# Optimization experiments

Measured on AMD Instinct MI355X. Metric: run time of the kernel, lower is better.

## Reference

```python
import jax, jax.numpy as jnp
import numpy as np

D_MODEL = 768
D_STATE = 128
EXPAND = 2
D_CONV = 4
HEADDIM = 48
D_INNER = EXPAND * D_MODEL            # 1536
NHEADS = D_INNER // HEADDIM           # 32
CONV_DIM = D_INNER + 2 * D_STATE      # 1792 (ngroups=1)
D_IN_PROJ = 2 * D_INNER + 2 * D_STATE + NHEADS  # 3360
EPS = 1e-5


def setup_inputs() -> dict:
    key = jax.random.key(0)
    ks = jax.random.split(key, 8)
    B, L = 2, 1024
    x = jax.random.normal(ks[0], (B, L, D_MODEL), dtype=jnp.float32)
    in_proj_w = jax.random.normal(ks[1], (D_IN_PROJ, D_MODEL), dtype=jnp.float32) * 0.02
    conv_w = jax.random.normal(ks[2], (CONV_DIM, D_CONV), dtype=jnp.float32) * 0.1
    conv_b = jnp.zeros((CONV_DIM,), dtype=jnp.float32)
    # dt init as in Mamba2: dt ~ logspace[1e-3, 1e-1], dt_bias = softplus^-1(dt)
    u = jax.random.uniform(ks[3], (NHEADS,), dtype=jnp.float32)
    dt = jnp.exp(u * (np.log(0.1) - np.log(0.001)) + np.log(0.001))
    dt_bias = jnp.log(jnp.expm1(dt))
    # A in [1, 16]
    A_log = jnp.log(jax.random.uniform(ks[4], (NHEADS,), dtype=jnp.float32) * 15.0 + 1.0)
    D = jnp.ones((NHEADS,), dtype=jnp.float32)
    rms_w = jnp.ones((D_INNER,), dtype=jnp.float32)
    out_proj_w = jax.random.normal(ks[5], (D_MODEL, D_INNER), dtype=jnp.float32) * 0.02
    ln_w = jnp.ones((D_MODEL,), dtype=jnp.float32)
    ln_b = jnp.zeros((D_MODEL,), dtype=jnp.float32)
    return {"x": x, "in_proj_w": in_proj_w, "conv_w": conv_w, "conv_b": conv_b,
            "dt_bias": dt_bias, "A_log": A_log, "D": D, "rms_w": rms_w,
            "out_proj_w": out_proj_w, "ln_w": ln_w, "ln_b": ln_b}


def _mamba_block(x, in_proj_w, conv_w, conv_b, dt_bias, A_log, D, rms_w, out_proj_w, ln_w, ln_b):
    B, L, _ = x.shape
    zxbcdt = jnp.einsum('bld,ed->ble', x, in_proj_w)          # (B,L,D_IN_PROJ)
    z = zxbcdt[..., :D_INNER]                                  # gate
    xBC = zxbcdt[..., D_INNER:D_INNER + CONV_DIM]              # (B,L,CONV_DIM)
    dt = jax.nn.softplus(zxbcdt[..., -NHEADS:] + dt_bias)      # (B,L,H)

    # causal depthwise conv1d (kernel 4) + SiLU
    xp = jnp.pad(xBC, ((0, 0), (D_CONV - 1, 0), (0, 0)))
    conv = conv_b
    for k in range(D_CONV):
        conv = conv + xp[:, k:k + L, :] * conv_w[:, k]
    xBC = jax.nn.silu(conv)

    xs = xBC[..., :D_INNER].reshape(B, L, NHEADS, HEADDIM)     # (B,L,H,P)
    Bm = xBC[..., D_INNER:D_INNER + D_STATE]                   # (B,L,N)
    Cm = xBC[..., D_INNER + D_STATE:]                          # (B,L,N)

    A = -jnp.exp(A_log)                                        # (H,)
    dA = jnp.exp(dt * A)                                       # (B,L,H)
    xdt = xs * dt[..., None]                                   # (B,L,H,P)

    def step(h, inp):
        dA_t, xdt_t, B_t, C_t = inp                            # (B,H),(B,H,P),(B,N),(B,N)
        h = h * dA_t[:, :, None, None] + jnp.einsum('bhp,bn->bhpn', xdt_t, B_t)
        y_t = jnp.einsum('bhpn,bn->bhp', h, C_t)
        return h, y_t

    h0 = jnp.zeros((B, NHEADS, HEADDIM, D_STATE), dtype=x.dtype)
    _, ys = jax.lax.scan(step, h0,
                         (dA.transpose(1, 0, 2), xdt.transpose(1, 0, 2, 3),
                          Bm.transpose(1, 0, 2), Cm.transpose(1, 0, 2)))
    y = ys.transpose(1, 0, 2, 3) + D[None, None, :, None] * xs  # (B,L,H,P)
    y = y.reshape(B, L, D_INNER)

    # gated RMSNorm: rmsnorm(y * silu(z)) * rms_w
    yg = y * jax.nn.silu(z)
    yg = yg * jax.lax.rsqrt(jnp.mean(yg * yg, axis=-1, keepdims=True) + EPS) * rms_w
    out = jnp.einsum('ble,de->bld', yg, out_proj_w)

    # residual + LayerNorm
    r = out + x
    mu = jnp.mean(r, axis=-1, keepdims=True)
    var = jnp.mean((r - mu) ** 2, axis=-1, keepdims=True)
    return (r - mu) * jax.lax.rsqrt(var + EPS) * ln_w + ln_b


def reference(x, in_proj_w, conv_w, conv_b, dt_bias, A_log, D, rms_w, out_proj_w, ln_w, ln_b):
    return _mamba_block(x, in_proj_w, conv_w, conv_b, dt_bias, A_log, D, rms_w,
                        out_proj_w, ln_w, ln_b)
```

## Files before the change

### kernel.cpp

```cpp
#include <hip/hip_runtime.h>
#include <math.h>

#define BDIM 2
#define LLEN 1024
#define DMODEL 768
#define DINNER 1536
#define DSTATE 128
#define NH 32
#define HD 48
#define CONVD 1792
#define DPROJ 3360
#define DPROJP 3456
#define QCH 128
#define NCH 8
#define ROWS (BDIM*LLEN)

typedef unsigned short ushort_t;
typedef __attribute__((ext_vector_type(4))) short short4v;
typedef __attribute__((ext_vector_type(8))) short short8v;
typedef __attribute__((ext_vector_type(4))) float floatx4;

#define OFF_ZX   0ull
#define OFF_XBC  3538944ull
#define OFF_DT   5373952ull
#define OFF_LA   5439488ull
#define OFF_SC   5505024ull
#define OFF_Y    8650752ull
#define OFF_PP   11796480ull
#define OFF_CBT  11797504ull
#define OFF_BTBF 12059648ull
#define OFF_XPT  12190720ull

__device__ __forceinline__ ushort_t f2bf(float f) {
  union { float f; unsigned int u; } v; v.f = f;
  return (ushort_t)((v.u + 0x7FFFu + ((v.u >> 16) & 1u)) >> 16);
}
__device__ __forceinline__ float bf2f(short s) {
  union { unsigned int u; float f; } v; v.u = ((unsigned int)(ushort_t)s) << 16;
  return v.f;
}

#define GLOAD_LDS16(gptr, lptr) \
  __builtin_amdgcn_global_load_lds( \
      (const __attribute__((address_space(1))) void*)(gptr), \
      (__attribute__((address_space(3))) void*)(lptr), 16, 0, 0)

__global__ __launch_bounds__(256) void convert_in_kernel(
    const float* __restrict__ x, const float* __restrict__ w,
    ushort_t* __restrict__ xbf, ushort_t* __restrict__ ipwbf) {
  const int blk = blockIdx.x;
  if (blk < 768) {
    const int i = blk * 256 + threadIdx.x;
    const float4 a = ((const float4*)x)[i * 2];
    const float4 b = ((const float4*)x)[i * 2 + 1];
    short8v o;
    o[0] = (short)f2bf(a.x); o[1] = (short)f2bf(a.y);
    o[2] = (short)f2bf(a.z); o[3] = (short)f2bf(a.w);
    o[4] = (short)f2bf(b.x); o[5] = (short)f2bf(b.y);
    o[6] = (short)f2bf(b.z); o[7] = (short)f2bf(b.w);
    *(short8v*)(xbf + (size_t)i * 8) = o;
  } else {
    const int i = (blk - 768) * 256 + threadIdx.x;
    const int row = i / (DMODEL / 8);
    short8v o;
    if (row < DPROJ) {
      const float4 a = ((const float4*)w)[i * 2];
      const float4 b = ((const float4*)w)[i * 2 + 1];
      o[0] = (short)f2bf(a.x); o[1] = (short)f2bf(a.y);
      o[2] = (short)f2bf(a.z); o[3] = (short)f2bf(a.w);
      o[4] = (short)f2bf(b.x); o[5] = (short)f2bf(b.y);
      o[6] = (short)f2bf(b.z); o[7] = (short)f2bf(b.w);
    } else {
      for (int j = 0; j < 8; j++) o[j] = 0;
    }
    *(short8v*)(ipwbf + (size_t)i * 8) = o;
  }
}

__global__ __launch_bounds__(256) void convert_bf16_kernel(
    const float* __restrict__ in, ushort_t* __restrict__ out, int n8) {
  const int i = blockIdx.x * 256 + threadIdx.x;
  if (i >= n8) return;
  const float4 a = ((const float4*)in)[i * 2];
  const float4 b = ((const float4*)in)[i * 2 + 1];
  short8v o;
  o[0] = (short)f2bf(a.x); o[1] = (short)f2bf(a.y);
  o[2] = (short)f2bf(a.z); o[3] = (short)f2bf(a.w);
  o[4] = (short)f2bf(b.x); o[5] = (short)f2bf(b.y);
  o[6] = (short)f2bf(b.z); o[7] = (short)f2bf(b.w);
  *(short8v*)(out + (size_t)i * 8) = o;
}

__global__ __launch_bounds__(256) void gemm_bf16_bfout(
    const ushort_t* __restrict__ A, const ushort_t* __restrict__ B,
    ushort_t* __restrict__ C, int M, int N, int K) {
  __shared__ __align__(16) ushort_t As[128 * 32];
  __shared__ __align__(16) ushort_t Bs[128 * 32];
  const int tid = threadIdx.x, lane = tid & 63, w = tid >> 6;
  const int wm = (w >> 1) * 64, wn = (w & 1) * 64;
  const int m0 = blockIdx.y * 128, n0 = blockIdx.x * 128;
  floatx4 acc[4][4];
#pragma unroll
  for (int i = 0; i < 4; i++)
#pragma unroll
    for (int j = 0; j < 4; j++) acc[i][j] = (floatx4){0.f, 0.f, 0.f, 0.f};
  const int srow = tid >> 2, skc = (tid & 3) * 8;
  const int kk = (lane >> 4) * 8, fr = lane & 15;
  for (int k0 = 0; k0 < K; k0 += 32) {
#pragma unroll
    for (int i = 0; i < 2; i++) {
      GLOAD_LDS16(A + (size_t)(m0 + i * 64 + srow) * K + k0 + skc,
                  As + (i * 64 + srow) * 32 + skc);
      GLOAD_LDS16(B + (size_t)(n0 + i * 64 + srow) * K + k0 + skc,
                  Bs + (i * 64 + srow) * 32 + skc);
    }
    __syncthreads();
    short8v a[4], bv[4];
#pragma unroll
    for (int mr = 0; mr < 4; mr++)
      a[mr] = *(const short8v*)(As + (wm + mr * 16 + fr) * 32 + kk);
#pragma unroll
    for (int nc = 0; nc < 4; nc++)
      bv[nc] = *(const short8v*)(Bs + (wn + nc * 16 + fr) * 32 + kk);
#pragma unroll
    for (int mr = 0; mr < 4; mr++)
#pragma unroll
      for (int nc = 0; nc < 4; nc++)
        acc[mr][nc] = __builtin_amdgcn_mfma_f32_16x16x32_bf16(
            a[mr], bv[nc], acc[mr][nc], 0, 0, 0);
    __syncthreads();
  }
  const int crow = (lane >> 4) * 4;
#pragma unroll
  for (int mr = 0; mr < 4; mr++)
#pragma unroll
    for (int nc = 0; nc < 4; nc++)
#pragma unroll
      for (int j = 0; j < 4; j++)
        C[(size_t)(m0 + wm + mr * 16 + crow + j) * N + n0 + wn + nc * 16 + fr] =
            f2bf(acc[mr][nc][j]);
}

__global__ __launch_bounds__(256) void gemm_bf16_n64(
    const ushort_t* __restrict__ A, const ushort_t* __restrict__ B,
    float* __restrict__ C, int M, int N, int K) {
  __shared__ __align__(16) ushort_t As[128 * 32];
  __shared__ __align__(16) ushort_t Bs[64 * 32];
  const int tid = threadIdx.x, lane = tid & 63, w = tid >> 6;
  const int wm = (w >> 1) * 64, wn = (w & 1) * 32;
  const int m0 = blockIdx.y * 128, n0 = blockIdx.x * 64;
  floatx4 acc[4][2];
#pragma unroll
  for (int i = 0; i < 4; i++)
#pragma unroll
    for (int j = 0; j < 2; j++) acc[i][j] = (floatx4){0.f, 0.f, 0.f, 0.f};
  const int srow = tid >> 2, skc = (tid & 3) * 8;
  const int kk = (lane >> 4) * 8, fr = lane & 15;
  for (int k0 = 0; k0 < K; k0 += 32) {
#pragma unroll
    for (int i = 0; i < 2; i++)
      GLOAD_LDS16(A + (size_t)(m0 + i * 64 + srow) * K + k0 + skc,
                  As + (i * 64 + srow) * 32 + skc);
    GLOAD_LDS16(B + (size_t)(n0 + srow) * K + k0 + skc, Bs + srow * 32 + skc);
    __syncthreads();
    short8v a[4], bv[2];
#pragma unroll
    for (int mr = 0; mr < 4; mr++)
      a[mr] = *(const short8v*)(As + (wm + mr * 16 + fr) * 32 + kk);
#pragma unroll
    for (int nc = 0; nc < 2; nc++)
      bv[nc] = *(const short8v*)(Bs + (wn + nc * 16 + fr) * 32 + kk);
#pragma unroll
    for (int mr = 0; mr < 4; mr++)
#pragma unroll
      for (int nc = 0; nc < 2; nc++)
        acc[mr][nc] = __builtin_amdgcn_mfma_f32_16x16x32_bf16(
            a[mr], bv[nc], acc[mr][nc], 0, 0, 0);
    __syncthreads();
  }
  const int crow = (lane >> 4) * 4;
#pragma unroll
  for (int mr = 0; mr < 4; mr++)
#pragma unroll
    for (int nc = 0; nc < 2; nc++)
#pragma unroll
      for (int j = 0; j < 4; j++)
        C[(size_t)(m0 + wm + mr * 16 + crow + j) * N + n0 + wn + nc * 16 + fr] =
            acc[mr][nc][j];
}

__global__ __launch_bounds__(256) void conv_dt_kernel(
    const ushort_t* __restrict__ zxb, const float* __restrict__ conv_w,
    const float* __restrict__ conv_b, const float* __restrict__ dt_bias,
    ushort_t* __restrict__ xbcb, float* __restrict__ dtbuf) {
  const int row = blockIdx.x;
  const int t = row % LLEN;
  const int tid = threadIdx.x;
  for (int g = tid; g < CONVD / 4; g += 256) {
    const int c = g * 4;
    const float4 cb = *(const float4*)&conv_b[c];
    float acc0 = cb.x, acc1 = cb.y, acc2 = cb.z, acc3 = cb.w;
    float4 cw[4];
#pragma unroll
    for (int j = 0; j < 4; j++) cw[j] = *(const float4*)&conv_w[(c + j) * 4];
#pragma unroll
    for (int k = 0; k < 4; k++) {
      if (t - 3 + k >= 0) {
        const short4v v = *(const short4v*)&zxb[(size_t)(row - 3 + k) * DPROJP + DINNER + c];
        acc0 += bf2f(v[0]) * ((const float*)&cw[0])[k];
        acc1 += bf2f(v[1]) * ((const float*)&cw[1])[k];
        acc2 += bf2f(v[2]) * ((const float*)&cw[2])[k];
        acc3 += bf2f(v[3]) * ((const float*)&cw[3])[k];
      }
    }
    short4v o;
    o[0] = (short)f2bf(acc0 / (1.f + expf(-acc0)));
    o[1] = (short)f2bf(acc1 / (1.f + expf(-acc1)));
    o[2] = (short)f2bf(acc2 / (1.f + expf(-acc2)));
    o[3] = (short)f2bf(acc3 / (1.f + expf(-acc3)));
    *(short4v*)&xbcb[(size_t)row * CONVD + c] = o;
  }
  if (tid < NH) {
    const float v = bf2f(zxb[(size_t)row * DPROJP + (DPROJ - NH) + tid]) + dt_bias[tid];
    dtbuf[row * NH + tid] = (v > 20.f) ? v : log1pf(expf(v));
  }
}

__global__ __launch_bounds__(128) void cumsum_kernel(
    const float* __restrict__ dtb, const float* __restrict__ A_log,
    float* __restrict__ la2, float* __restrict__ Pp) {
  const int c = blockIdx.x, h = blockIdx.y, b = blockIdx.z;
  const int tid = threadIdx.x, lane = tid & 63;
  const int row = b * LLEN + c * QCH + tid;
  __shared__ float s0;
  float v = dtb[(size_t)row * NH + h];
#pragma unroll
  for (int off = 1; off < 64; off <<= 1) {
    const float u = __shfl_up(v, off, 64);
    if (lane >= off) v += u;
  }
  if (tid == 63) s0 = v;
  __syncthreads();
  if (tid >= 64) v += s0;
  const float la2v = -expf(A_log[h]) * v * 1.44269504088896f;
  la2[(size_t)row * NH + h] = la2v;
  if (tid == 127) Pp[(b * NH + h) * NCH + c] = exp2f(la2v);
}

__global__ __launch_bounds__(256) void prep_bt_kernel(
    const ushort_t* __restrict__ xbcb, ushort_t* __restrict__ BTbf) {
  const int bc = blockIdx.x;
  const int b = bc / NCH, c = bc % NCH;
  const int row0 = b * LLEN + c * QCH;
  const int tid = threadIdx.x;
  __shared__ ushort_t lb[128][136];
  for (int idx = tid; idx < 128 * 32; idx += 256) {
    const int t = idx >> 5, f4 = (idx & 31) * 4;
    const short4v v = *(const short4v*)&xbcb[(size_t)(row0 + t) * CONVD + DINNER + f4];
    *(short4v*)&lb[t][f4] = v;
  }
  __syncthreads();
  for (int idx = tid; idx < 128 * 16; idx += 256) {
    const int n = idx & 127, t0 = (idx >> 7) * 8;
    short8v o;
#pragma unroll
    for (int j = 0; j < 8; j++) o[j] = lb[t0 + j][n];
    *(short8v*)&BTbf[(size_t)(bc * 128 + n) * 128 + t0] = o;
  }
}

__global__ __launch_bounds__(256) void prep_x_kernel(
    const ushort_t* __restrict__ xbcb, const float* __restrict__ dtb,
    ushort_t* __restrict__ XpT) {
  const int c = blockIdx.x, h = blockIdx.y, b = blockIdx.z;
  const int row0 = b * LLEN + c * QCH;
  const int tid = threadIdx.x;
  __shared__ ushort_t xl[128][56];
  __shared__ float dts[128];
  if (tid < 128) dts[tid] = dtb[(size_t)(row0 + tid) * NH + h];
  __syncthreads();
  for (int idx = tid; idx < 128 * 12; idx += 256) {
    const int r = idx / 12, f4 = (idx % 12) * 4;
    const short4v v = *(const short4v*)&xbcb[(size_t)(row0 + r) * CONVD + h * HD + f4];
    const float d = dts[r];
    short4v o;
    o[0] = (short)f2bf(bf2f(v[0]) * d); o[1] = (short)f2bf(bf2f(v[1]) * d);
    o[2] = (short)f2bf(bf2f(v[2]) * d); o[3] = (short)f2bf(bf2f(v[3]) * d);
    *(short4v*)&xl[r][f4] = o;
  }
  __syncthreads();
  const size_t base = ((size_t)(b * NCH + c) * NH + h) * HD * 128;
  for (int idx = tid; idx < 48 * 16; idx += 256) {
    const int p = idx % 48, t0 = (idx / 48) * 8;
    short8v o;
#pragma unroll
    for (int j = 0; j < 8; j++) o[j] = xl[t0 + j][p];
    *(short8v*)&XpT[base + (size_t)p * 128 + t0] = o;
  }
}

__global__ __launch_bounds__(256) void cbt_kernel(
    const ushort_t* __restrict__ xbcb, float* __restrict__ CBt) {
  const int bc = blockIdx.x;
  const int b = bc / NCH, c = bc % NCH;
  const int row0 = b * LLEN + c * QCH;
  const int tid = threadIdx.x, lane = tid & 63, w = tid >> 6;
  const int wm = w * 32;
  const int fr = lane & 15, kk = (lane >> 4) * 8;
  floatx4 acc[2][8];
#pragma unroll
  for (int i = 0; i < 2; i++)
#pragma unroll
    for (int j = 0; j < 8; j++) acc[i][j] = (floatx4){0.f, 0.f, 0.f, 0.f};
  for (int ki = 0; ki < 4; ki++) {
    const int kg = ki * 32 + kk;
    short8v a[2], bv[8];
#pragma unroll
    for (int mt = 0; mt < 2; mt++)
      a[mt] = *(const short8v*)&xbcb[(size_t)(row0 + wm + mt * 16 + fr) * CONVD +
                                     DINNER + DSTATE + kg];
#pragma unroll
    for (int nt = 0; nt < 8; nt++)
      bv[nt] = *(const short8v*)&xbcb[(size_t)(row0 + nt * 16 + fr) * CONVD +
                                      DINNER + kg];
#pragma unroll
    for (int mt = 0; mt < 2; mt++)
#pragma unroll
      for (int nt = 0; nt < 8; nt++)
        acc[mt][nt] = __builtin_amdgcn_mfma_f32_16x16x32_bf16(
            a[mt], bv[nt], acc[mt][nt], 0, 0, 0);
  }
  const int crow = (lane >> 4) * 4;
#pragma unroll
  for (int mt = 0; mt < 2; mt++)
#pragma unroll
    for (int nt = 0; nt < 8; nt++)
#pragma unroll
      for (int j = 0; j < 4; j++)
        CBt[(size_t)(bc * 128 + wm + mt * 16 + crow + j) * 128 + nt * 16 + fr] =
            acc[mt][nt][j];
}

__global__ __launch_bounds__(256) void stateA_kernel(
    const ushort_t* __restrict__ XpT, const ushort_t* __restrict__ BTbf,
    const float* __restrict__ la2, float* __restrict__ Sc) {
  const int c = blockIdx.x, h = blockIdx.y, b = blockIdx.z;
  const int bc = b * NCH + c, bh = b * NH + h;
  const int row0 = b * LLEN + c * QCH;
  const int tid = threadIdx.x, lane = tid & 63, w = tid >> 6;
  __shared__ float ew[128];
  const float laL = la2[(size_t)(row0 + 127) * NH + h];
  if (tid < 128) ew[tid] = exp2f(laL - la2[(size_t)(row0 + tid) * NH + h]);
  __syncthreads();
  const int wn = w * 32;
  const int fr = lane & 15, kk = (lane >> 4) * 8;
  const size_t xbase = ((size_t)bc * NH + h) * HD * 128;
  floatx4 acc[3][2];
#pragma unroll
  for (int i = 0; i < 3; i++)
#pragma unroll
    for (int j = 0; j < 2; j++) acc[i][j] = (floatx4){0.f, 0.f, 0.f, 0.f};
  for (int ki = 0; ki < 4; ki++) {
    const int kg = ki * 32 + kk;
    short8v a[3], bv[2];
#pragma unroll
    for (int mt = 0; mt < 3; mt++) {
      const short8v raw = *(const short8v*)&XpT[xbase + (size_t)(mt * 16 + fr) * 128 + kg];
      short8v s;
#pragma unroll
      for (int e = 0; e < 8; e++) s[e] = (short)f2bf(bf2f(raw[e]) * ew[kg + e]);
      a[mt] = s;
    }
#pragma unroll
    for (int nt = 0; nt < 2; nt++)
      bv[nt] = *(const short8v*)&BTbf[(size_t)(bc * 128 + wn + nt * 16 + fr) * 128 + kg];
#pragma unroll
    for (int mt = 0; mt < 3; mt++)
#pragma unroll
      for (int nt = 0; nt < 2; nt++)
        acc[mt][nt] = __builtin_amdgcn_mfma_f32_16x16x32_bf16(
            a[mt], bv[nt], acc[mt][nt], 0, 0, 0);
  }
  const int crow = (lane >> 4) * 4;
  float* sc = Sc + (size_t)(bh * NCH + c) * (HD * DSTATE);
#pragma unroll
  for (int mt = 0; mt < 3; mt++)
#pragma unroll
    for (int nt = 0; nt < 2; nt++)
#pragma unroll
      for (int j = 0; j < 4; j++)
        sc[(size_t)(mt * 16 + crow + j) * 128 + wn + nt * 16 + fr] = acc[mt][nt][j];
}

__global__ __launch_bounds__(256) void chunk_combine_kernel(
    float* __restrict__ Sc, const float* __restrict__ Pp) {
  const int bh = blockIdx.x;
  const int tid = threadIdx.x;
  for (int e = tid; e < HD * DSTATE; e += 256) {
    float hv = 0.f;
#pragma unroll
    for (int c = 0; c < NCH; c++) {
      const size_t idx = ((size_t)(bh * NCH + c)) * HD * DSTATE + e;
      const float sv = Sc[idx];
      Sc[idx] = hv;
      hv = hv * Pp[bh * NCH + c] + sv;
    }
  }
}

__global__ __launch_bounds__(256) void ykernel(
    const float* __restrict__ CBt, const ushort_t* __restrict__ XpT,
    const ushort_t* __restrict__ xbcb, const float* __restrict__ Hc,
    const float* __restrict__ la2, float* __restrict__ y) {
  const int c = blockIdx.x, h = blockIdx.y, b = blockIdx.z;
  const int bc = b * NCH + c, bh = b * NH + h;
  const int row0 = b * LLEN + c * QCH;
  const int tid = threadIdx.x, lane = tid & 63, w = tid >> 6;
  __shared__ float laL[128], el[128];
  if (tid < 128) {
    const float v = la2[(size_t)(row0 + tid) * NH + h];
    laL[tid] = v; el[tid] = exp2f(v);
  }
  __syncthreads();
  const int wm = w * 32;
  const int fr = lane & 15, kk = (lane >> 4) * 8;
  const size_t xbase = ((size_t)bc * NH + h) * HD * 128;
  const float* hin = Hc + (size_t)(bh * NCH + c) * (HD * DSTATE);
  floatx4 acc[2][3];
#pragma unroll
  for (int i = 0; i < 2; i++)
#pragma unroll
    for (int j = 0; j < 3; j++) acc[i][j] = (floatx4){0.f, 0.f, 0.f, 0.f};

  for (int ki = 0; ki < 4; ki++) {
    const int kg = ki * 32 + kk;
    short8v a[2], bv[3];
#pragma unroll
    for (int mt = 0; mt < 2; mt++) {
      const int t = wm + mt * 16 + fr;
      const float lt = laL[t];
      const float* cb = &CBt[(size_t)(bc * 128 + t) * 128 + kg];
      const float4 u0 = *(const float4*)cb;
      const float4 u1 = *(const float4*)(cb + 4);
      const float f[8] = {u0.x, u0.y, u0.z, u0.w, u1.x, u1.y, u1.z, u1.w};
      short8v s;
#pragma unroll
      for (int e = 0; e < 8; e++) {
        const int sidx = kg + e;
        const float m = (t >= sidx) ? exp2f(lt - laL[sidx]) : 0.f;
        s[e] = (short)f2bf(f[e] * m);
      }
      a[mt] = s;
    }
#pragma unroll
    for (int nt = 0; nt < 3; nt++)
      bv[nt] = *(const short8v*)&XpT[xbase + (size_t)(nt * 16 + fr) * 128 + kg];
#pragma unroll
    for (int mt = 0; mt < 2; mt++)
#pragma unroll
      for (int nt = 0; nt < 3; nt++)
        acc[mt][nt] = __builtin_amdgcn_mfma_f32_16x16x32_bf16(
            a[mt], bv[nt], acc[mt][nt], 0, 0, 0);
  }
  for (int ki = 0; ki < 4; ki++) {
    const int kg = ki * 32 + kk;
    short8v a[2], bv[3];
#pragma unroll
    for (int mt = 0; mt < 2; mt++) {
      const int t = wm + mt * 16 + fr;
      const float scl = el[t];
      const short8v raw = *(const short8v*)&xbcb[(size_t)(row0 + t) * CONVD +
                                                 DINNER + DSTATE + kg];
      short8v s;
#pragma unroll
      for (int e = 0; e < 8; e++) s[e] = (short)f2bf(bf2f(raw[e]) * scl);
      a[mt] = s;
    }
#pragma unroll
    for (int nt = 0; nt < 3; nt++) {
      const float* hp = &hin[(size_t)(nt * 16 + fr) * 128 + kg];
      const float4 u0 = *(const float4*)hp;
      const float4 u1 = *(const float4*)(hp + 4);
      const float f[8] = {u0.x, u0.y, u0.z, u0.w, u1.x, u1.y, u1.z, u1.w};
      short8v s;
#pragma unroll
      for (int e = 0; e < 8; e++) s[e] = (short)f2bf(f[e]);
      bv[nt] = s;
    }
#pragma unroll
    for (int mt = 0; mt < 2; mt++)
#pragma unroll
      for (int nt = 0; nt < 3; nt++)
        acc[mt][nt] = __builtin_amdgcn_mfma_f32_16x16x32_bf16(
            a[mt], bv[nt], acc[mt][nt], 0, 0, 0);
  }
  const int crow = (lane >> 4) * 4;
#pragma unroll
  for (int mt = 0; mt < 2; mt++)
#pragma unroll
    for (int nt = 0; nt < 3; nt++)
#pragma unroll
      for (int j = 0; j < 4; j++) {
        const int row = row0 + wm + mt * 16 + crow + j;
        y[(size_t)row * DINNER + h * HD + nt * 16 + fr] = acc[mt][nt][j];
      }
}

__global__ __launch_bounds__(256) void gate_rms_kernel(
    const ushort_t* __restrict__ zxb, const ushort_t* __restrict__ xbcb,
    const float* __restrict__ Dv, const float* __restrict__ rms_w,
    const float* __restrict__ y, ushort_t* __restrict__ ybf) {
  const int row = blockIdx.x;
  const int tid = threadIdx.x;
  __shared__ float sred[4];
  float g[8];
  float ss = 0.f;
  if (tid < 192) {
    const int e0 = tid * 8;
    const short8v xv = *(const short8v*)&xbcb[(size_t)row * CONVD + e0];
    const short8v zv = *(const short8v*)&zxb[(size_t)row * DPROJP + e0];
    const float4 y0 = *(const float4*)&y[(size_t)row * DINNER + e0];
    const float4 y1 = *(const float4*)&y[(size_t)row * DINNER + e0 + 4];
    const float yf[8] = {y0.x, y0.y, y0.z, y0.w, y1.x, y1.y, y1.z, y1.w};
#pragma unroll
    for (int j = 0; j < 8; j++) {
      const int e = e0 + j;
      const float yv = yf[j] + Dv[e / HD] * bf2f(xv[j]);
      const float z = bf2f(zv[j]);
      const float gv = yv * (z / (1.f + expf(-z)));
      g[j] = gv;
      ss += gv * gv;
    }
  } else {
#pragma unroll
    for (int j = 0; j < 8; j++) g[j] = 0.f;
  }
#pragma unroll
  for (int off = 32; off; off >>= 1) ss += __shfl_down(ss, off, 64);
  if ((tid & 63) == 0) sred[tid >> 6] = ss;
  __syncthreads();
  const float tot = sred[0] + sred[1] + sred[2] + sred[3];
  const float scale = rsqrtf(tot / DINNER + 1e-5f);
  if (tid < 192) {
    const int e0 = tid * 8;
    const float4 w0 = *(const float4*)&rms_w[e0];
    const float4 w1 = *(const float4*)&rms_w[e0 + 4];
    const float wf[8] = {w0.x, w0.y, w0.z, w0.w, w1.x, w1.y, w1.z, w1.w};
    short8v o;
#pragma unroll
    for (int j = 0; j < 8; j++) o[j] = (short)f2bf(g[j] * scale * wf[j]);
    *(short8v*)&ybf[(size_t)row * DINNER + e0] = o;
  }
}

__global__ __launch_bounds__(256) void resid_ln_kernel(
    const float* __restrict__ go, const float* __restrict__ x,
    const float* __restrict__ ln_w, const float* __restrict__ ln_b,
    float* __restrict__ out) {
  const int row = blockIdx.x;
  const int tid = threadIdx.x;
  __shared__ float sred[4];
  __shared__ float sred2[4];
  float r[3];
  float s = 0.f;
#pragma unroll
  for (int i = 0; i < 3; i++) {
    const int e = tid + i * 256;
    r[i] = go[(size_t)row * DMODEL + e] + x[(size_t)row * DMODEL + e];
    s += r[i];
  }
#pragma unroll
  for (int off = 32; off; off >>= 1) s += __shfl_down(s, off, 64);
  if ((tid & 63) == 0) sred[tid >> 6] = s;
  __syncthreads();
  const float mu = (sred[0] + sred[1] + sred[2] + sred[3]) * (1.f / DMODEL);
  float s2 = 0.f;
#pragma unroll
  for (int i = 0; i < 3; i++) {
    const float d = r[i] - mu;
    s2 += d * d;
  }
#pragma unroll
  for (int off = 32; off; off >>= 1) s2 += __shfl_down(s2, off, 64);
  if ((tid & 63) == 0) sred2[tid >> 6] = s2;
  __syncthreads();
  const float var = (sred2[0] + sred2[1] + sred2[2] + sred2[3]) * (1.f / DMODEL);
  const float inv = rsqrtf(var + 1e-5f);
#pragma unroll
  for (int i = 0; i < 3; i++) {
    const int e = tid + i * 256;
    out[(size_t)row * DMODEL + e] = (r[i] - mu) * inv * ln_w[e] + ln_b[e];
  }
}

extern "C" void kernel_launch(void* const* d_in, const int* in_sizes, int n_in,
                              void* d_out, int out_size, void* d_ws, size_t ws_size,
                              hipStream_t stream) {
  const float* x          = (const float*)d_in[0];
  const float* in_proj_w  = (const float*)d_in[1];
  const float* conv_w     = (const float*)d_in[2];
  const float* conv_b     = (const float*)d_in[3];
  const float* dt_bias    = (const float*)d_in[4];
  const float* A_log      = (const float*)d_in[5];
  const float* Dv         = (const float*)d_in[6];
  const float* rms_w      = (const float*)d_in[7];
  const float* out_proj_w = (const float*)d_in[8];
  const float* ln_w       = (const float*)d_in[9];
  const float* ln_b       = (const float*)d_in[10];
  float* out = (float*)d_out;
  float* ws  = (float*)d_ws;

  ushort_t* zxb  = (ushort_t*)(ws + OFF_ZX);
  ushort_t* xbcb = (ushort_t*)(ws + OFF_XBC);
  float* dtb  = ws + OFF_DT;
  float* la2  = ws + OFF_LA;
  float* Sc   = ws + OFF_SC;
  float* ybuf = ws + OFF_Y;
  float* Pp   = ws + OFF_PP;
  float* CBt  = ws + OFF_CBT;
  ushort_t* BTbf = (ushort_t*)(ws + OFF_BTBF);
  ushort_t* XpT  = (ushort_t*)(ws + OFF_XPT);

  ushort_t* xbf   = (ushort_t*)(ws + OFF_Y);
  ushort_t* ipwbf = (ushort_t*)(ws + OFF_Y + 786432);
  ushort_t* ybf   = (ushort_t*)(ws + OFF_SC);
  ushort_t* opwbf = (ushort_t*)(ws + OFF_SC + 1572864);
  float*    go    = ws + OFF_ZX;

  convert_in_kernel<<<2064, 256, 0, stream>>>(x, in_proj_w, xbf, ipwbf);

  gemm_bf16_bfout<<<dim3(DPROJP / 128, ROWS / 128), 256, 0, stream>>>(
      xbf, ipwbf, zxb, ROWS, DPROJP, DMODEL);

  conv_dt_kernel<<<ROWS, 256, 0, stream>>>(zxb, conv_w, conv_b, dt_bias, xbcb, dtb);

  cumsum_kernel<<<dim3(NCH, NH, BDIM), 128, 0, stream>>>(dtb, A_log, la2, Pp);
  prep_bt_kernel<<<BDIM * NCH, 256, 0, stream>>>(xbcb, BTbf);
  prep_x_kernel<<<dim3(NCH, NH, BDIM), 256, 0, stream>>>(xbcb, dtb, XpT);
  cbt_kernel<<<BDIM * NCH, 256, 0, stream>>>(xbcb, CBt);
  stateA_kernel<<<dim3(NCH, NH, BDIM), 256, 0, stream>>>(XpT, BTbf, la2, Sc);
  chunk_combine_kernel<<<BDIM * NH, 256, 0, stream>>>(Sc, Pp);
  ykernel<<<dim3(NCH, NH, BDIM), 256, 0, stream>>>(CBt, XpT, xbcb, Sc, la2, ybuf);

  gate_rms_kernel<<<ROWS, 256, 0, stream>>>(zxb, xbcb, Dv, rms_w, ybuf, ybf);

  convert_bf16_kernel<<<(DMODEL * DINNER / 8 + 255) / 256, 256, 0, stream>>>(
      out_proj_w, opwbf, DMODEL * DINNER / 8);
  gemm_bf16_n64<<<dim3(DMODEL / 64, ROWS / 128), 256, 0, stream>>>(
      ybf, opwbf, go, ROWS, DMODEL, DINNER);

  resid_ln_kernel<<<ROWS, 256, 0, stream>>>(go, x, ln_w, ln_b, out);
}
```

Measured before the change: 234.4 us.

## Merge small SSD prep kernels, fold weight conversion, widen chunk combine

Several small launches are merged into block-indexed multi-role kernels. The out_proj weight conversion joins the input conversion kernel, and cumsum, prep_x and prep_bt become one kernel. cbt runs inside stateA's grid, and chunk_combine is split into 8 slices per head for more parallelism. The y buffer is stored as bf16 instead of fp32 to halve that traffic, and the workspace is re-laid out so the buffers no longer alias. This cuts launch overhead and idle tail time, at the cost of some precision in y.

```diff
diff --git a/kernel.cpp b/kernel.cpp
--- a/kernel.cpp
+++ b/kernel.cpp
@@ -26,10 +26,15 @@
 #define OFF_LA   5439488ull
 #define OFF_SC   5505024ull
 #define OFF_Y    8650752ull
-#define OFF_PP   11796480ull
-#define OFF_CBT  11797504ull
-#define OFF_BTBF 12059648ull
-#define OFF_XPT  12190720ull
+#define OFF_PP   10223616ull
+#define OFF_CBT  10224640ull
+#define OFF_BTBF 10486784ull
+#define OFF_XPT  10617856ull
+#define OFF_XBF  12190720ull
+#define OFF_IPW  12977152ull
+#define OFF_OPW  14304256ull
+#define OFF_YBF  14894080ull
+#define OFF_GO   16466944ull
 
 __device__ __forceinline__ ushort_t f2bf(float f) {
   union { float f; unsigned int u; } v; v.f = f;
@@ -47,7 +52,8 @@
 
 __global__ __launch_bounds__(256) void convert_in_kernel(
     const float* __restrict__ x, const float* __restrict__ w,
-    ushort_t* __restrict__ xbf, ushort_t* __restrict__ ipwbf) {
+    const float* __restrict__ opw, ushort_t* __restrict__ xbf,
+    ushort_t* __restrict__ ipwbf, ushort_t* __restrict__ opwbf) {
   const int blk = blockIdx.x;
   if (blk < 768) {
     const int i = blk * 256 + threadIdx.x;
@@ -59,7 +65,7 @@
     o[4] = (short)f2bf(b.x); o[5] = (short)f2bf(b.y);
     o[6] = (short)f2bf(b.z); o[7] = (short)f2bf(b.w);
     *(short8v*)(xbf + (size_t)i * 8) = o;
-  } else {
+  } else if (blk < 2064) {
     const int i = (blk - 768) * 256 + threadIdx.x;
     const int row = i / (DMODEL / 8);
     short8v o;
@@ -74,21 +80,17 @@
       for (int j = 0; j < 8; j++) o[j] = 0;
     }
     *(short8v*)(ipwbf + (size_t)i * 8) = o;
-  }
-}
-
-__global__ __launch_bounds__(256) void convert_bf16_kernel(
-    const float* __restrict__ in, ushort_t* __restrict__ out, int n8) {
-  const int i = blockIdx.x * 256 + threadIdx.x;
-  if (i >= n8) return;
-  const float4 a = ((const float4*)in)[i * 2];
-  const float4 b = ((const float4*)in)[i * 2 + 1];
-  short8v o;
-  o[0] = (short)f2bf(a.x); o[1] = (short)f2bf(a.y);
-  o[2] = (short)f2bf(a.z); o[3] = (short)f2bf(a.w);
-  o[4] = (short)f2bf(b.x); o[5] = (short)f2bf(b.y);
-  o[6] = (short)f2bf(b.z); o[7] = (short)f2bf(b.w);
-  *(short8v*)(out + (size_t)i * 8) = o;
+  } else {
+    const int i = (blk - 2064) * 256 + threadIdx.x;
+    const float4 a = ((const float4*)opw)[i * 2];
+    const float4 b = ((const float4*)opw)[i * 2 + 1];
+    short8v o;
+    o[0] = (short)f2bf(a.x); o[1] = (short)f2bf(a.y);
+    o[2] = (short)f2bf(a.z); o[3] = (short)f2bf(a.w);
+    o[4] = (short)f2bf(b.x); o[5] = (short)f2bf(b.y);
+    o[6] = (short)f2bf(b.z); o[7] = (short)f2bf(b.w);
+    *(short8v*)(opwbf + (size_t)i * 8) = o;
+  }
 }
 
 __global__ __launch_bounds__(256) void gemm_bf16_bfout(
@@ -226,177 +228,177 @@
   }
 }
 
-__global__ __launch_bounds__(128) void cumsum_kernel(
-    const float* __restrict__ dtb, const float* __restrict__ A_log,
-    float* __restrict__ la2, float* __restrict__ Pp) {
-  const int c = blockIdx.x, h = blockIdx.y, b = blockIdx.z;
-  const int tid = threadIdx.x, lane = tid & 63;
-  const int row = b * LLEN + c * QCH + tid;
-  __shared__ float s0;
-  float v = dtb[(size_t)row * NH + h];
-#pragma unroll
-  for (int off = 1; off < 64; off <<= 1) {
-    const float u = __shfl_up(v, off, 64);
-    if (lane >= off) v += u;
-  }
-  if (tid == 63) s0 = v;
-  __syncthreads();
-  if (tid >= 64) v += s0;
-  const float la2v = -expf(A_log[h]) * v * 1.44269504088896f;
-  la2[(size_t)row * NH + h] = la2v;
-  if (tid == 127) Pp[(b * NH + h) * NCH + c] = exp2f(la2v);
-}
-
-__global__ __launch_bounds__(256) void prep_bt_kernel(
-    const ushort_t* __restrict__ xbcb, ushort_t* __restrict__ BTbf) {
-  const int bc = blockIdx.x;
-  const int b = bc / NCH, c = bc % NCH;
-  const int row0 = b * LLEN + c * QCH;
+__global__ __launch_bounds__(256) void prepfuse_kernel(
+    const ushort_t* __restrict__ xbcb, const float* __restrict__ dtb,
+    const float* __restrict__ A_log, ushort_t* __restrict__ XpT,
+    ushort_t* __restrict__ BTbf, float* __restrict__ la2,
+    float* __restrict__ Pp) {
+  __shared__ ushort_t lb[128][136];
+  __shared__ float dts[128];
+  const int blk = blockIdx.x;
   const int tid = threadIdx.x;
-  __shared__ ushort_t lb[128][136];
-  for (int idx = tid; idx < 128 * 32; idx += 256) {
-    const int t = idx >> 5, f4 = (idx & 31) * 4;
-    const short4v v = *(const short4v*)&xbcb[(size_t)(row0 + t) * CONVD + DINNER + f4];
-    *(short4v*)&lb[t][f4] = v;
-  }
-  __syncthreads();
-  for (int idx = tid; idx < 128 * 16; idx += 256) {
-    const int n = idx & 127, t0 = (idx >> 7) * 8;
-    short8v o;
-#pragma unroll
-    for (int j = 0; j < 8; j++) o[j] = lb[t0 + j][n];
-    *(short8v*)&BTbf[(size_t)(bc * 128 + n) * 128 + t0] = o;
-  }
-}
-
-__global__ __launch_bounds__(256) void prep_x_kernel(
-    const ushort_t* __restrict__ xbcb, const float* __restrict__ dtb,
-    ushort_t* __restrict__ XpT) {
-  const int c = blockIdx.x, h = blockIdx.y, b = blockIdx.z;
-  const int row0 = b * LLEN + c * QCH;
-  const int tid = threadIdx.x;
-  __shared__ ushort_t xl[128][56];
-  __shared__ float dts[128];
-  if (tid < 128) dts[tid] = dtb[(size_t)(row0 + tid) * NH + h];
-  __syncthreads();
-  for (int idx = tid; idx < 128 * 12; idx += 256) {
-    const int r = idx / 12, f4 = (idx % 12) * 4;
-    const short4v v = *(const short4v*)&xbcb[(size_t)(row0 + r) * CONVD + h * HD + f4];
-    const float d = dts[r];
-    short4v o;
-    o[0] = (short)f2bf(bf2f(v[0]) * d); o[1] = (short)f2bf(bf2f(v[1]) * d);
-    o[2] = (short)f2bf(bf2f(v[2]) * d); o[3] = (short)f2bf(bf2f(v[3]) * d);
-    *(short4v*)&xl[r][f4] = o;
-  }
-  __syncthreads();
-  const size_t base = ((size_t)(b * NCH + c) * NH + h) * HD * 128;
-  for (int idx = tid; idx < 48 * 16; idx += 256) {
-    const int p = idx % 48, t0 = (idx / 48) * 8;
-    short8v o;
-#pragma unroll
-    for (int j = 0; j < 8; j++) o[j] = xl[t0 + j][p];
-    *(short8v*)&XpT[base + (size_t)p * 128 + t0] = o;
-  }
-}
-
-__global__ __launch_bounds__(256) void cbt_kernel(
-    const ushort_t* __restrict__ xbcb, float* __restrict__ CBt) {
-  const int bc = blockIdx.x;
-  const int b = bc / NCH, c = bc % NCH;
-  const int row0 = b * LLEN + c * QCH;
+  if (blk < 512) {
+    const int c = blk & 7, h = (blk >> 3) & 31, b = blk >> 8;
+    const int row0 = b * LLEN + c * QCH;
+    if (tid < 128) dts[tid] = dtb[(size_t)(row0 + tid) * NH + h];
+    __syncthreads();
+    for (int idx = tid; idx < 128 * 12; idx += 256) {
+      const int r = idx / 12, f4 = (idx % 12) * 4;
+      const short4v v = *(const short4v*)&xbcb[(size_t)(row0 + r) * CONVD + h * HD + f4];
+      const float d = dts[r];
+      short4v o;
+      o[0] = (short)f2bf(bf2f(v[0]) * d); o[1] = (short)f2bf(bf2f(v[1]) * d);
+      o[2] = (short)f2bf(bf2f(v[2]) * d); o[3] = (short)f2bf(bf2f(v[3]) * d);
+      *(short4v*)&lb[r][f4] = o;
+    }
+    __syncthreads();
+    const size_t base = ((size_t)(b * NCH + c) * NH + h) * HD * 128;
+    for (int idx = tid; idx < 48 * 16; idx += 256) {
+      const int p = idx % 48, t0 = (idx / 48) * 8;
+      short8v o;
+#pragma unroll
+      for (int j = 0; j < 8; j++) o[j] = lb[t0 + j][p];
+      *(short8v*)&XpT[base + (size_t)p * 128 + t0] = o;
+    }
+  } else if (blk < 528) {
+    const int bc = blk - 512;
+    const int b = bc / NCH, c = bc % NCH;
+    const int row0 = b * LLEN + c * QCH;
+    for (int idx = tid; idx < 128 * 32; idx += 256) {
+      const int t = idx >> 5, f4 = (idx & 31) * 4;
+      const short4v v = *(const short4v*)&xbcb[(size_t)(row0 + t) * CONVD + DINNER + f4];
+      *(short4v*)&lb[t][f4] = v;
+    }
+    __syncthreads();
+    for (int idx = tid; idx < 128 * 16; idx += 256) {
+      const int n = idx & 127, t0 = (idx >> 7) * 8;
+      short8v o;
+#pragma unroll
+      for (int j = 0; j < 8; j++) o[j] = lb[t0 + j][n];
+      *(short8v*)&BTbf[(size_t)(bc * 128 + n) * 128 + t0] = o;
+    }
+  } else {
+    const int idx = blk - 528;
+    const int c = idx & 7, h = (idx >> 3) & 31, b = idx >> 8;
+    const int lane = tid & 63;
+    const int row = b * LLEN + c * QCH + tid;
+    float v = 0.f;
+    if (tid < 128) v = dtb[(size_t)row * NH + h];
+#pragma unroll
+    for (int off = 1; off < 64; off <<= 1) {
+      const float u = __shfl_up(v, off, 64);
+      if (lane >= off) v += u;
+    }
+    if (tid == 63) dts[0] = v;
+    __syncthreads();
+    if (tid >= 64 && tid < 128) v += dts[0];
+    if (tid < 128) {
+      const float la2v = -expf(A_log[h]) * v * 1.44269504088896f;
+      la2[(size_t)row * NH + h] = la2v;
+      if (tid == 127) Pp[(b * NH + h) * NCH + c] = exp2f(la2v);
+    }
+  }
+}
+
+__global__ __launch_bounds__(256) void stateA_cbt_kernel(
+    const ushort_t* __restrict__ XpT, const ushort_t* __restrict__ BTbf,
+    const ushort_t* __restrict__ xbcb, const float* __restrict__ la2,
+    float* __restrict__ Sc, float* __restrict__ CBt) {
+  __shared__ float ew[128];
+  const int blk = blockIdx.x;
   const int tid = threadIdx.x, lane = tid & 63, w = tid >> 6;
-  const int wm = w * 32;
   const int fr = lane & 15, kk = (lane >> 4) * 8;
-  floatx4 acc[2][8];
-#pragma unroll
-  for (int i = 0; i < 2; i++)
-#pragma unroll
-    for (int j = 0; j < 8; j++) acc[i][j] = (floatx4){0.f, 0.f, 0.f, 0.f};
-  for (int ki = 0; ki < 4; ki++) {
-    const int kg = ki * 32 + kk;
-    short8v a[2], bv[8];
+  if (blk < 512) {
+    const int c = blk & 7, h = (blk >> 3) & 31, b = blk >> 8;
+    const int bc = b * NCH + c, bh = b * NH + h;
+    const int row0 = b * LLEN + c * QCH;
+    const float laL = la2[(size_t)(row0 + 127) * NH + h];
+    if (tid < 128) ew[tid] = exp2f(laL - la2[(size_t)(row0 + tid) * NH + h]);
+    __syncthreads();
+    const int wn = w * 32;
+    const size_t xbase = ((size_t)bc * NH + h) * HD * 128;
+    floatx4 acc[3][2];
+#pragma unroll
+    for (int i = 0; i < 3; i++)
+#pragma unroll
+      for (int j = 0; j < 2; j++) acc[i][j] = (floatx4){0.f, 0.f, 0.f, 0.f};
+    for (int ki = 0; ki < 4; ki++) {
+      const int kg = ki * 32 + kk;
+      short8v a[3], bv[2];
+#pragma unroll
+      for (int mt = 0; mt < 3; mt++) {
+        const short8v raw = *(const short8v*)&XpT[xbase + (size_t)(mt * 16 + fr) * 128 + kg];
+        short8v s;
+#pragma unroll
+        for (int e = 0; e < 8; e++) s[e] = (short)f2bf(bf2f(raw[e]) * ew[kg + e]);
+        a[mt] = s;
+      }
+#pragma unroll
+      for (int nt = 0; nt < 2; nt++)
+        bv[nt] = *(const short8v*)&BTbf[(size_t)(bc * 128 + wn + nt * 16 + fr) * 128 + kg];
+#pragma unroll
+      for (int mt = 0; mt < 3; mt++)
+#pragma unroll
+        for (int nt = 0; nt < 2; nt++)
+          acc[mt][nt] = __builtin_amdgcn_mfma_f32_16x16x32_bf16(
+              a[mt], bv[nt], acc[mt][nt], 0, 0, 0);
+    }
+    const int crow = (lane >> 4) * 4;
+    float* sc = Sc + (size_t)(bh * NCH + c) * (HD * DSTATE);
+#pragma unroll
+    for (int mt = 0; mt < 3; mt++)
+#pragma unroll
+      for (int nt = 0; nt < 2; nt++)
+#pragma unroll
+        for (int j = 0; j < 4; j++)
+          sc[(size_t)(mt * 16 + crow + j) * 128 + wn + nt * 16 + fr] = acc[mt][nt][j];
+  } else {
+    const int bc = blk - 512;
+    const int b = bc / NCH, c = bc % NCH;
+    const int row0 = b * LLEN + c * QCH;
+    const int wm = w * 32;
+    floatx4 acc[2][8];
+#pragma unroll
+    for (int i = 0; i < 2; i++)
+#pragma unroll
+      for (int j = 0; j < 8; j++) acc[i][j] = (floatx4){0.f, 0.f, 0.f, 0.f};
+    for (int ki = 0; ki < 4; ki++) {
+      const int kg = ki * 32 + kk;
+      short8v a[2], bv[8];
+#pragma unroll
+      for (int mt = 0; mt < 2; mt++)
+        a[mt] = *(const short8v*)&xbcb[(size_t)(row0 + wm + mt * 16 + fr) * CONVD +
+                                       DINNER + DSTATE + kg];
+#pragma unroll
+      for (int nt = 0; nt < 8; nt++)
+        bv[nt] = *(const short8v*)&xbcb[(size_t)(row0 + nt * 16 + fr) * CONVD +
+                                        DINNER + kg];
+#pragma unroll
+      for (int mt = 0; mt < 2; mt++)
+#pragma unroll
+        for (int nt = 0; nt < 8; nt++)
+          acc[mt][nt] = __builtin_amdgcn_mfma_f32_16x16x32_bf16(
+              a[mt], bv[nt], acc[mt][nt], 0, 0, 0);
+    }
+    const int crow = (lane >> 4) * 4;
 #pragma unroll
     for (int mt = 0; mt < 2; mt++)
-      a[mt] = *(const short8v*)&xbcb[(size_t)(row0 + wm + mt * 16 + fr) * CONVD +
-                                     DINNER + DSTATE + kg];
-#pragma unroll
-    for (int nt = 0; nt < 8; nt++)
-      bv[nt] = *(const short8v*)&xbcb[(size_t)(row0 + nt * 16 + fr) * CONVD +
-                                      DINNER + kg];
-#pragma unroll
-    for (int mt = 0; mt < 2; mt++)
 #pragma unroll
       for (int nt = 0; nt < 8; nt++)
-        acc[mt][nt] = __builtin_amdgcn_mfma_f32_16x16x32_bf16(
-            a[mt], bv[nt], acc[mt][nt], 0, 0, 0);
-  }
-  const int crow = (lane >> 4) * 4;
-#pragma unroll
-  for (int mt = 0; mt < 2; mt++)
-#pragma unroll
-    for (int nt = 0; nt < 8; nt++)
-#pragma unroll
-      for (int j = 0; j < 4; j++)
-        CBt[(size_t)(bc * 128 + wm + mt * 16 + crow + j) * 128 + nt * 16 + fr] =
-            acc[mt][nt][j];
-}
-
-__global__ __launch_bounds__(256) void stateA_kernel(
-    const ushort_t* __restrict__ XpT, const ushort_t* __restrict__ BTbf,
-    const float* __restrict__ la2, float* __restrict__ Sc) {
-  const int c = blockIdx.x, h = blockIdx.y, b = blockIdx.z;
-  const int bc = b * NCH + c, bh = b * NH + h;
-  const int row0 = b * LLEN + c * QCH;
-  const int tid = threadIdx.x, lane = tid & 63, w = tid >> 6;
-  __shared__ float ew[128];
-  const float laL = la2[(size_t)(row0 + 127) * NH + h];
-  if (tid < 128) ew[tid] = exp2f(laL - la2[(size_t)(row0 + tid) * NH + h]);
-  __syncthreads();
-  const int wn = w * 32;
-  const int fr = lane & 15, kk = (lane >> 4) * 8;
-  const size_t xbase = ((size_t)bc * NH + h) * HD * 128;
-  floatx4 acc[3][2];
-#pragma unroll
-  for (int i = 0; i < 3; i++)
-#pragma unroll
-    for (int j = 0; j < 2; j++) acc[i][j] = (floatx4){0.f, 0.f, 0.f, 0.f};
-  for (int ki = 0; ki < 4; ki++) {
-    const int kg = ki * 32 + kk;
-    short8v a[3], bv[2];
-#pragma unroll
-    for (int mt = 0; mt < 3; mt++) {
-      const short8v raw = *(const short8v*)&XpT[xbase + (size_t)(mt * 16 + fr) * 128 + kg];
-      short8v s;
-#pragma unroll
-      for (int e = 0; e < 8; e++) s[e] = (short)f2bf(bf2f(raw[e]) * ew[kg + e]);
-      a[mt] = s;
-    }
-#pragma unroll
-    for (int nt = 0; nt < 2; nt++)
-      bv[nt] = *(const short8v*)&BTbf[(size_t)(bc * 128 + wn + nt * 16 + fr) * 128 + kg];
-#pragma unroll
-    for (int mt = 0; mt < 3; mt++)
-#pragma unroll
-      for (int nt = 0; nt < 2; nt++)
-        acc[mt][nt] = __builtin_amdgcn_mfma_f32_16x16x32_bf16(
-            a[mt], bv[nt], acc[mt][nt], 0, 0, 0);
-  }
-  const int crow = (lane >> 4) * 4;
-  float* sc = Sc + (size_t)(bh * NCH + c) * (HD * DSTATE);
-#pragma unroll
-  for (int mt = 0; mt < 3; mt++)
-#pragma unroll
-    for (int nt = 0; nt < 2; nt++)
-#pragma unroll
-      for (int j = 0; j < 4; j++)
-        sc[(size_t)(mt * 16 + crow + j) * 128 + wn + nt * 16 + fr] = acc[mt][nt][j];
+#pragma unroll
+        for (int j = 0; j < 4; j++)
+          CBt[(size_t)(bc * 128 + wm + mt * 16 + crow + j) * 128 + nt * 16 + fr] =
+              acc[mt][nt][j];
+  }
 }
 
 __global__ __launch_bounds__(256) void chunk_combine_kernel(
     float* __restrict__ Sc, const float* __restrict__ Pp) {
-  const int bh = blockIdx.x;
+  const int bh = blockIdx.x >> 3;
+  const int slice = blockIdx.x & 7;
   const int tid = threadIdx.x;
-  for (int e = tid; e < HD * DSTATE; e += 256) {
+  const int e0 = slice * 768;
+  for (int e = e0 + tid; e < e0 + 768; e += 256) {
     float hv = 0.f;
 #pragma unroll
     for (int c = 0; c < NCH; c++) {
@@ -411,7 +413,7 @@
 __global__ __launch_bounds__(256) void ykernel(
     const float* __restrict__ CBt, const ushort_t* __restrict__ XpT,
     const ushort_t* __restrict__ xbcb, const float* __restrict__ Hc,
-    const float* __restrict__ la2, float* __restrict__ y) {
+    const float* __restrict__ la2, ushort_t* __restrict__ yb) {
   const int c = blockIdx.x, h = blockIdx.y, b = blockIdx.z;
   const int bc = b * NCH + c, bh = b * NH + h;
   const int row0 = b * LLEN + c * QCH;
@@ -502,14 +504,14 @@
 #pragma unroll
       for (int j = 0; j < 4; j++) {
         const int row = row0 + wm + mt * 16 + crow + j;
-        y[(size_t)row * DINNER + h * HD + nt * 16 + fr] = acc[mt][nt][j];
+        yb[(size_t)row * DINNER + h * HD + nt * 16 + fr] = f2bf(acc[mt][nt][j]);
       }
 }
 
 __global__ __launch_bounds__(256) void gate_rms_kernel(
     const ushort_t* __restrict__ zxb, const ushort_t* __restrict__ xbcb,
     const float* __restrict__ Dv, const float* __restrict__ rms_w,
-    const float* __restrict__ y, ushort_t* __restrict__ ybf) {
+    const ushort_t* __restrict__ yb, ushort_t* __restrict__ ybf) {
   const int row = blockIdx.x;
   const int tid = threadIdx.x;
   __shared__ float sred[4];
@@ -519,15 +521,13 @@
     const int e0 = tid * 8;
     const short8v xv = *(const short8v*)&xbcb[(size_t)row * CONVD + e0];
     const short8v zv = *(const short8v*)&zxb[(size_t)row * DPROJP + e0];
-    const float4 y0 = *(const float4*)&y[(size_t)row * DINNER + e0];
-    const float4 y1 = *(const float4*)&y[(size_t)row * DINNER + e0 + 4];
-    const float yf[8] = {y0.x, y0.y, y0.z, y0.w, y1.x, y1.y, y1.z, y1.w};
+    const short8v yv = *(const short8v*)&yb[(size_t)row * DINNER + e0];
 #pragma unroll
     for (int j = 0; j < 8; j++) {
       const int e = e0 + j;
-      const float yv = yf[j] + Dv[e / HD] * bf2f(xv[j]);
+      const float yf = bf2f(yv[j]) + Dv[e / HD] * bf2f(xv[j]);
       const float z = bf2f(zv[j]);
-      const float gv = yv * (z / (1.f + expf(-z)));
+      const float gv = yf * (z / (1.f + expf(-z)));
       g[j] = gv;
       ss += gv * gv;
     }
@@ -610,44 +610,33 @@
   float* out = (float*)d_out;
   float* ws  = (float*)d_ws;
 
-  ushort_t* zxb  = (ushort_t*)(ws + OFF_ZX);
-  ushort_t* xbcb = (ushort_t*)(ws + OFF_XBC);
+  ushort_t* zxb   = (ushort_t*)(ws + OFF_ZX);
+  ushort_t* xbcb  = (ushort_t*)(ws + OFF_XBC);
   float* dtb  = ws + OFF_DT;
   float* la2  = ws + OFF_LA;
   float* Sc   = ws + OFF_SC;
-  float* ybuf = ws + OFF_Y;
+  ushort_t* ybuf = (ushort_t*)(ws + OFF_Y);
   float* Pp   = ws + OFF_PP;
   float* CBt  = ws + OFF_CBT;
-  ushort_t* BTbf = (ushort_t*)(ws + OFF_BTBF);
-  ushort_t* XpT  = (ushort_t*)(ws + OFF_XPT);
-
-  ushort_t* xbf   = (ushort_t*)(ws + OFF_Y);
-  ushort_t* ipwbf = (ushort_t*)(ws + OFF_Y + 786432);
-  ushort_t* ybf   = (ushort_t*)(ws + OFF_SC);
-  ushort_t* opwbf = (ushort_t*)(ws + OFF_SC + 1572864);
-  float*    go    = ws + OFF_ZX;
-
-  convert_in_kernel<<<2064, 256, 0, stream>>>(x, in_proj_w, xbf, ipwbf);
-
+  ushort_t* BTbf  = (ushort_t*)(ws + OFF_BTBF);
+  ushort_t* XpT   = (ushort_t*)(ws + OFF_XPT);
+  ushort_t* xbf   = (ushort_t*)(ws + OFF_XBF);
+  ushort_t* ipwbf = (ushort_t*)(ws + OFF_IPW);
+  ushort_t* opwbf = (ushort_t*)(ws + OFF_OPW);
+  ushort_t* ybf   = (ushort_t*)(ws + OFF_YBF);
+  float*    go    = ws + OFF_GO;
+
+  convert_in_kernel<<<2640, 256, 0, stream>>>(x, in_proj_w, out_proj_w,
+                                              xbf, ipwbf, opwbf);
   gemm_bf16_bfout<<<dim3(DPROJP / 128, ROWS / 128), 256, 0, stream>>>(
       xbf, ipwbf, zxb, ROWS, DPROJP, DMODEL);
-
   conv_dt_kernel<<<ROWS, 256, 0, stream>>>(zxb, conv_w, conv_b, dt_bias, xbcb, dtb);
-
-  cumsum_kernel<<<dim3(NCH, NH, BDIM), 128, 0, stream>>>(dtb, A_log, la2, Pp);
-  prep_bt_kernel<<<BDIM * NCH, 256, 0, stream>>>(xbcb, BTbf);
-  prep_x_kernel<<<dim3(NCH, NH, BDIM), 256, 0, stream>>>(xbcb, dtb, XpT);
-  cbt_kernel<<<BDIM * NCH, 256, 0, stream>>>(xbcb, CBt);
-  stateA_kernel<<<dim3(NCH, NH, BDIM), 256, 0, stream>>>(XpT, BTbf, la2, Sc);
-  chunk_combine_kernel<<<BDIM * NH, 256, 0, stream>>>(Sc, Pp);
+  prepfuse_kernel<<<1040, 256, 0, stream>>>(xbcb, dtb, A_log, XpT, BTbf, la2, Pp);
+  stateA_cbt_kernel<<<528, 256, 0, stream>>>(XpT, BTbf, xbcb, la2, Sc, CBt);
+  chunk_combine_kernel<<<512, 256, 0, stream>>>(Sc, Pp);
   ykernel<<<dim3(NCH, NH, BDIM), 256, 0, stream>>>(CBt, XpT, xbcb, Sc, la2, ybuf);
-
   gate_rms_kernel<<<ROWS, 256, 0, stream>>>(zxb, xbcb, Dv, rms_w, ybuf, ybf);
-
-  convert_bf16_kernel<<<(DMODEL * DINNER / 8 + 255) / 256, 256, 0, stream>>>(
-      out_proj_w, opwbf, DMODEL * DINNER / 8);
   gemm_bf16_n64<<<dim3(DMODEL / 64, ROWS / 128), 256, 0, stream>>>(
       ybf, opwbf, go, ROWS, DMODEL, DINNER);
-
   resid_ln_kernel<<<ROWS, 256, 0, stream>>>(go, x, ln_w, ln_b, out);
 }
```

Measured after the change: 210.0 us. 10.4% less time.
